# Performance work log

Hardware: AMD Instinct MI355X
Metric: run time of the kernel (lower is better)

Reference implementation:

```python
import jax, jax.numpy as jnp
import numpy as np

N_GLIMPSES = 3
GS = 64          # glimpse_size
IN_C = 3         # input_channels
B, H, W = 64, 512, 512


def get_glimpses(image, loc):
    """Multi-scale glimpse extraction (tf.image.extract_glimpse, centered+normalized)
    followed by antialiased bicubic resize to GS x GS, concatenated on channels."""
    b, h, w, c = image.shape
    max_size = GS * 2 ** (N_GLIMPSES - 1)
    padded = jnp.pad(image, ((0, 0), (max_size, max_size), (max_size, max_size), (0, 0)))
    hp, wp = h + 2 * max_size, w + 2 * max_size
    # normalized+centered offsets: (-1,-1)=upper-left, (1,1)=lower-right of padded image
    center = (loc + 1.0) * 0.5 * jnp.array([hp, wp], dtype=jnp.float32)  # (y, x) per batch
    glimpses = []
    for i in range(N_GLIMPSES):
        s = GS * 2 ** i  # current crop size (python int, static)
        tl = jnp.round(center - 0.5 * s).astype(jnp.int32)
        tl = jnp.clip(tl, 0, jnp.array([hp - s, wp - s], dtype=jnp.int32))

        def slice_one(img, yx):
            return jax.lax.dynamic_slice(img, (yx[0], yx[1], 0), (s, s, c))

        g = jax.vmap(slice_one)(padded, tl)                      # [B, s, s, C]
        g = jax.image.resize(g, (b, GS, GS, c), method='cubic')  # antialiased bicubic
        glimpses.append(g)
    return jnp.concatenate(glimpses, axis=-1)  # [B, GS, GS, N_GLIMPSES*C]


def setup_inputs() -> dict:
    key = jax.random.key(0)
    ks = jax.random.split(key, 10)
    image = jax.random.uniform(ks[0], (B, H, W, IN_C), dtype=jnp.float32)
    loc = jax.random.uniform(ks[1], (B, 2), dtype=jnp.float32, minval=-1.0, maxval=1.0)
    cg = N_GLIMPSES * IN_C
    # conv1_g: full-kernel (GS x GS) valid conv -> 1x1x128
    Wg = jax.random.normal(ks[2], (GS, GS, cg, 128), dtype=jnp.float32) * (1.0 / np.sqrt(GS * GS * cg))
    bg = jnp.zeros((128,), jnp.float32)
    # conv1_l: 1x1 conv on loc [B,1,1,2]
    Wl = jax.random.normal(ks[3], (2, 128), dtype=jnp.float32) * (1.0 / np.sqrt(2.0))
    bl = jnp.zeros((128,), jnp.float32)
    # out: 1x1 conv 128 -> 256
    Wo = jax.random.normal(ks[4], (128, 256), dtype=jnp.float32) * (1.0 / np.sqrt(128.0))
    bo = jnp.zeros((256,), jnp.float32)
    return {"image": image, "loc": loc, "Wg": Wg, "bg": bg, "Wl": Wl, "bl": bl, "Wo": Wo, "bo": bo}


def reference(image, loc, Wg, bg, Wl, bl, Wo, bo):
    glimpses = get_glimpses(image, loc)  # [B, GS, GS, N_GLIMPSES*IN_C]
    # conv1_g with kernel == glimpse size and VALID padding == dense contraction over hwc
    x1 = jax.nn.relu(jnp.einsum('bhwc,hwck->bk', glimpses, Wg) + bg)  # [B,128]
    x2 = jax.nn.relu(loc @ Wl + bl)                                   # [B,128]
    out = jax.nn.relu((x1 + x2) @ Wo + bo)                            # [B,256]
    return out
```

## Files before the change

kernel.cpp:

```cpp
#include <hip/hip_runtime.h>

#define IMG_H 512
#define IMG_W 512
#define PAD   256
#define HP    1024
#define BATCH 64
#define KTOT  36864
#define KTILE 144
#define KB    16
#define NTILES 256

__device__ __forceinline__ float keys_cubic(float x) {
  if (x >= 2.0f) return 0.0f;
  if (x >= 1.0f) return ((-0.5f * x + 2.5f) * x - 4.0f) * x + 2.0f;
  return ((1.5f * x - 2.5f) * x) * x + 1.0f;
}

template <int KS>
__device__ __forceinline__ void glimpse_resize_body(
    const float* __restrict__ imb, int b, int y, int tly, int tlx,
    float* __restrict__ G, int tid, float* tmp) {
  constexpr int S  = 64 * KS;
  constexpr int NT = 4 * KS;
  const float fks = (float)KS;

  float sy  = ((float)y + 0.5f) * fks - 0.5f;
  int   iy0 = (int)ceilf(sy - 2.0f * fks);
  float wy[NT];
  float wsum = 0.0f;
#pragma unroll
  for (int t = 0; t < NT; ++t) {
    int i = iy0 + t;
    float w = 0.0f;
    if (i >= 0 && i < S) w = keys_cubic(fabsf(sy - (float)i) / fks);
    wy[t] = w;
    wsum += w;
  }
  float winv = 1.0f / wsum;
#pragma unroll
  for (int t = 0; t < NT; ++t) wy[t] *= winv;

  for (int e = tid; e < S * 3; e += 256) {
    int xcol = e / 3;
    int c    = e - 3 * xcol;
    int px   = tlx - PAD + xcol;
    float a = 0.0f;
    if ((unsigned)px < (unsigned)IMG_W) {
      const float* colp = imb + (px * 3 + c);
#pragma unroll
      for (int t = 0; t < NT; ++t) {
        int py = tly + iy0 + t - PAD;
        if ((unsigned)py < (unsigned)IMG_H)
          a = fmaf(wy[t], colp[py * (IMG_W * 3)], a);
      }
    }
    tmp[e] = a;
  }
  __syncthreads();

  if (tid < 192) {
    int xo = tid / 3;
    int c  = tid - 3 * xo;
    float sx  = ((float)xo + 0.5f) * fks - 0.5f;
    int   ix0 = (int)ceilf(sx - 2.0f * fks);
    float a = 0.0f, wsx = 0.0f;
#pragma unroll
    for (int t = 0; t < NT; ++t) {
      int i = ix0 + t;
      if (i >= 0 && i < S) {
        float w = keys_cubic(fabsf(sx - (float)i) / fks);
        wsx += w;
        a = fmaf(w, tmp[i * 3 + c], a);
      }
    }
    constexpr int sc = (KS == 2) ? 1 : 2;
    G[(((size_t)b * 64 + y) * 64 + xo) * 9 + 3 * sc + c] = a / wsx;
  }
}

__global__ __launch_bounds__(256) void glimpse_kernel(
    const float* __restrict__ img, const float* __restrict__ loc,
    float* __restrict__ G) {
  __shared__ float tmp[768];
  int blk = blockIdx.x;
  int y   = blk & 63;
  int t3  = blk >> 6;
  int sc  = t3 % 3;
  int b   = t3 / 3;
  int tid = threadIdx.x;

  float cy = (loc[2 * b] + 1.0f) * 0.5f * 1024.0f;
  float cx = (loc[2 * b + 1] + 1.0f) * 0.5f * 1024.0f;
  int s   = 64 << sc;
  int tly = min(max((int)rintf(cy - 0.5f * (float)s), 0), HP - s);
  int tlx = min(max((int)rintf(cx - 0.5f * (float)s), 0), HP - s);
  const float* imb = img + (size_t)b * (IMG_H * IMG_W * 3);

  if (sc == 0) {
    if (tid < 192) {
      int x = tid / 3, c = tid - 3 * (tid / 3);
      int py = tly + y - PAD, px = tlx + x - PAD;
      float v = 0.0f;
      if ((unsigned)py < (unsigned)IMG_H && (unsigned)px < (unsigned)IMG_W)
        v = imb[(py * IMG_W + px) * 3 + c];
      G[(((size_t)b * 64 + y) * 64 + x) * 9 + c] = v;
    }
  } else if (sc == 1) {
    glimpse_resize_body<2>(imb, b, y, tly, tlx, G, tid, tmp);
  } else {
    glimpse_resize_body<4>(imb, b, y, tly, tlx, G, tid, tmp);
  }
}

__global__ __launch_bounds__(256) void gemm_kernel(
    const float* __restrict__ G, const float* __restrict__ Wg,
    float* __restrict__ partials) {
  const int tile = blockIdx.x;
  const int tid  = threadIdx.x;
  const int tn   = tid & 15;
  const int tm   = tid >> 4;
  __shared__ float Gs[2][KB][64];
  __shared__ float Ws[2][KB][128];

  const int gb = tid >> 2;
  const int gj = (tid & 3) * 4;
  const int wr = tid >> 4;
  const int wc = (tid & 15) * 8;
  const size_t gbase = (size_t)gb * KTOT + (size_t)tile * KTILE + gj;
  const size_t wbase = ((size_t)tile * KTILE + wr) * 128 + wc;

  float4 g4 = *(const float4*)(G + gbase);
  float4 wa = *(const float4*)(Wg + wbase);
  float4 wb = *(const float4*)(Wg + wbase + 4);

  float acc[4][8];
#pragma unroll
  for (int mi = 0; mi < 4; ++mi)
#pragma unroll
    for (int ni = 0; ni < 8; ++ni) acc[mi][ni] = 0.0f;

  constexpr int NCHUNK = KTILE / KB;
#pragma unroll
  for (int chunk = 0; chunk < NCHUNK; ++chunk) {
    const int buf = chunk & 1;
    Gs[buf][gj + 0][gb] = g4.x;
    Gs[buf][gj + 1][gb] = g4.y;
    Gs[buf][gj + 2][gb] = g4.z;
    Gs[buf][gj + 3][gb] = g4.w;
    *(float4*)&Ws[buf][wr][wc]     = wa;
    *(float4*)&Ws[buf][wr][wc + 4] = wb;
    __syncthreads();
    if (chunk + 1 < NCHUNK) {
      g4 = *(const float4*)(G + gbase + (chunk + 1) * KB);
      wa = *(const float4*)(Wg + wbase + (size_t)(chunk + 1) * KB * 128);
      wb = *(const float4*)(Wg + wbase + (size_t)(chunk + 1) * KB * 128 + 4);
    }
#pragma unroll
    for (int j = 0; j < KB; ++j) {
      float4 gv = *(const float4*)&Gs[buf][j][tm * 4];
      float4 w0 = *(const float4*)&Ws[buf][j][tn * 8];
      float4 w1 = *(const float4*)&Ws[buf][j][tn * 8 + 4];
      float gm[4] = {gv.x, gv.y, gv.z, gv.w};
      float wn[8] = {w0.x, w0.y, w0.z, w0.w, w1.x, w1.y, w1.z, w1.w};
#pragma unroll
      for (int mi = 0; mi < 4; ++mi)
#pragma unroll
        for (int ni = 0; ni < 8; ++ni)
          acc[mi][ni] = fmaf(gm[mi], wn[ni], acc[mi][ni]);
    }
  }

#pragma unroll
  for (int mi = 0; mi < 4; ++mi) {
    int m = tm * 4 + mi;
    float* dst = partials + ((size_t)m * NTILES + tile) * 128 + tn * 8;
    *(float4*)dst       = make_float4(acc[mi][0], acc[mi][1], acc[mi][2], acc[mi][3]);
    *(float4*)(dst + 4) = make_float4(acc[mi][4], acc[mi][5], acc[mi][6], acc[mi][7]);
  }
}

__global__ __launch_bounds__(256) void finalize_kernel(
    const float* __restrict__ partials, const float* __restrict__ loc,
    const float* __restrict__ bg, const float* __restrict__ Wl,
    const float* __restrict__ bl, const float* __restrict__ Wo,
    const float* __restrict__ bo, float* __restrict__ out) {
  int b   = blockIdx.x;
  int tid = threadIdx.x;
  int k    = tid & 127;
  int half = tid >> 7;

  const float* base = partials + (size_t)b * NTILES * 128;
  float s = 0.0f;
  for (int t = half; t < NTILES; t += 2)
    s += base[t * 128 + k];

  __shared__ float red[256];
  __shared__ float h[128];
  red[tid] = s;
  __syncthreads();
  if (tid < 128) {
    float ss = red[tid] + red[tid + 128];
    float x1 = fmaxf(ss + bg[tid], 0.0f);
    float x2 = fmaxf(fmaf(loc[2 * b], Wl[tid],
                          fmaf(loc[2 * b + 1], Wl[128 + tid], bl[tid])),
                     0.0f);
    h[tid] = x1 + x2;
  }
  __syncthreads();
  {
    int n = tid;
    float a = bo[n];
#pragma unroll 8
    for (int kk = 0; kk < 128; ++kk) a = fmaf(h[kk], Wo[kk * 256 + n], a);
    out[(size_t)b * 256 + n] = fmaxf(a, 0.0f);
  }
}

extern "C" void kernel_launch(void* const* d_in, const int* in_sizes, int n_in,
                              void* d_out, int out_size, void* d_ws, size_t ws_size,
                              hipStream_t stream) {
  const float* img = (const float*)d_in[0];
  const float* loc = (const float*)d_in[1];
  const float* Wg  = (const float*)d_in[2];
  const float* bg  = (const float*)d_in[3];
  const float* Wl  = (const float*)d_in[4];
  const float* bl  = (const float*)d_in[5];
  const float* Wo  = (const float*)d_in[6];
  const float* bo  = (const float*)d_in[7];
  float* out = (float*)d_out;

  float* ws = (float*)d_ws;
  float* G        = ws;
  float* partials = ws + 2359296;

  glimpse_kernel<<<BATCH * 3 * 64, 256, 0, stream>>>(img, loc, G);
  gemm_kernel<<<NTILES, 256, 0, stream>>>(G, Wg, partials);
  finalize_kernel<<<BATCH, 256, 0, stream>>>(partials, loc, bg, Wl, bl, Wo, bo, out);
}
```

Measured before the change: 344.1 us.

## Merge three glimpse scales into one block per row and vectorize finalize reduction

The glimpse kernel now handles all three scales for one (batch, row) in a single block instead of launching a separate block per scale. This cuts the block count threefold, shares the location and top-left computation, and keeps threads busy across scales that were previously imbalanced. The finalize kernel now reads the per-tile partial sums with float4 loads and reduces them in shared memory across 8 groups. In exchange, each glimpse block does more serial work and uses more shared memory, which may lower occupancy.

```diff
diff --git a/kernel.cpp b/kernel.cpp
--- a/kernel.cpp
+++ b/kernel.cpp
@@ -16,99 +16,138 @@
   return ((1.5f * x - 2.5f) * x) * x + 1.0f;
 }
 
-template <int KS>
-__device__ __forceinline__ void glimpse_resize_body(
-    const float* __restrict__ imb, int b, int y, int tly, int tlx,
-    float* __restrict__ G, int tid, float* tmp) {
-  constexpr int S  = 64 * KS;
-  constexpr int NT = 4 * KS;
-  const float fks = (float)KS;
-
-  float sy  = ((float)y + 0.5f) * fks - 0.5f;
-  int   iy0 = (int)ceilf(sy - 2.0f * fks);
-  float wy[NT];
-  float wsum = 0.0f;
-#pragma unroll
-  for (int t = 0; t < NT; ++t) {
-    int i = iy0 + t;
-    float w = 0.0f;
-    if (i >= 0 && i < S) w = keys_cubic(fabsf(sy - (float)i) / fks);
-    wy[t] = w;
-    wsum += w;
-  }
-  float winv = 1.0f / wsum;
-#pragma unroll
-  for (int t = 0; t < NT; ++t) wy[t] *= winv;
-
-  for (int e = tid; e < S * 3; e += 256) {
-    int xcol = e / 3;
-    int c    = e - 3 * xcol;
-    int px   = tlx - PAD + xcol;
+__device__ __forceinline__ int iclamp(int v, int lo, int hi) {
+  return min(max(v, lo), hi);
+}
+
+__global__ __launch_bounds__(256) void glimpse_kernel(
+    const float* __restrict__ img, const float* __restrict__ loc,
+    float* __restrict__ G) {
+  __shared__ float tmp1[384];
+  __shared__ float tmp2[768];
+  const int y   = blockIdx.x & 63;
+  const int b   = blockIdx.x >> 6;
+  const int tid = threadIdx.x;
+
+  const float cy = (loc[2 * b] + 1.0f) * 0.5f * 1024.0f;
+  const float cx = (loc[2 * b + 1] + 1.0f) * 0.5f * 1024.0f;
+  const int tly0 = iclamp((int)rintf(cy - 32.0f), 0, HP - 64);
+  const int tlx0 = iclamp((int)rintf(cx - 32.0f), 0, HP - 64);
+  const int tly1 = iclamp((int)rintf(cy - 64.0f), 0, HP - 128);
+  const int tlx1 = iclamp((int)rintf(cx - 64.0f), 0, HP - 128);
+  const int tly2 = iclamp((int)rintf(cy - 128.0f), 0, HP - 256);
+  const int tlx2 = iclamp((int)rintf(cx - 128.0f), 0, HP - 256);
+  const float* imb  = img + (size_t)b * (IMG_H * IMG_W * 3);
+  float*       Grow = G + ((size_t)b * 64 + y) * (64 * 9);
+
+  if (tid < 192) {
+    int x = tid / 3, c = tid - 3 * (tid / 3);
+    int py = tly0 + y - PAD, px = tlx0 + x - PAD;
+    float v = 0.0f;
+    if ((unsigned)py < (unsigned)IMG_H && (unsigned)px < (unsigned)IMG_W)
+      v = imb[(py * IMG_W + px) * 3 + c];
+    Grow[x * 9 + c] = v;
+  }
+
+  float wy1[8];
+  int iy0_1;
+  {
+    float sy = ((float)y + 0.5f) * 2.0f - 0.5f;
+    iy0_1 = (int)ceilf(sy - 4.0f);
+    float ws = 0.0f;
+#pragma unroll
+    for (int t = 0; t < 8; ++t) {
+      int i = iy0_1 + t;
+      float w = (i >= 0 && i < 128) ? keys_cubic(fabsf(sy - (float)i) * 0.5f) : 0.0f;
+      wy1[t] = w;
+      ws += w;
+    }
+    float wi = 1.0f / ws;
+#pragma unroll
+    for (int t = 0; t < 8; ++t) wy1[t] *= wi;
+  }
+  float wy2[16];
+  int iy0_2;
+  {
+    float sy = ((float)y + 0.5f) * 4.0f - 0.5f;
+    iy0_2 = (int)ceilf(sy - 8.0f);
+    float ws = 0.0f;
+#pragma unroll
+    for (int t = 0; t < 16; ++t) {
+      int i = iy0_2 + t;
+      float w = (i >= 0 && i < 256) ? keys_cubic(fabsf(sy - (float)i) * 0.25f) : 0.0f;
+      wy2[t] = w;
+      ws += w;
+    }
+    float wi = 1.0f / ws;
+#pragma unroll
+    for (int t = 0; t < 16; ++t) wy2[t] *= wi;
+  }
+
+  for (int e = tid; e < 384; e += 256) {
+    int x = e / 3, c = e - 3 * (e / 3);
+    int px = tlx1 - PAD + x;
     float a = 0.0f;
     if ((unsigned)px < (unsigned)IMG_W) {
       const float* colp = imb + (px * 3 + c);
 #pragma unroll
-      for (int t = 0; t < NT; ++t) {
-        int py = tly + iy0 + t - PAD;
+      for (int t = 0; t < 8; ++t) {
+        int py = tly1 + iy0_1 + t - PAD;
         if ((unsigned)py < (unsigned)IMG_H)
-          a = fmaf(wy[t], colp[py * (IMG_W * 3)], a);
-      }
-    }
-    tmp[e] = a;
+          a = fmaf(wy1[t], colp[py * (IMG_W * 3)], a);
+      }
+    }
+    tmp1[e] = a;
+  }
+  for (int e = tid; e < 768; e += 256) {
+    int x = e / 3, c = e - 3 * (e / 3);
+    int px = tlx2 - PAD + x;
+    float a = 0.0f;
+    if ((unsigned)px < (unsigned)IMG_W) {
+      const float* colp = imb + (px * 3 + c);
+#pragma unroll
+      for (int t = 0; t < 16; ++t) {
+        int py = tly2 + iy0_2 + t - PAD;
+        if ((unsigned)py < (unsigned)IMG_H)
+          a = fmaf(wy2[t], colp[py * (IMG_W * 3)], a);
+      }
+    }
+    tmp2[e] = a;
   }
   __syncthreads();
 
-  if (tid < 192) {
-    int xo = tid / 3;
-    int c  = tid - 3 * xo;
-    float sx  = ((float)xo + 0.5f) * fks - 0.5f;
-    int   ix0 = (int)ceilf(sx - 2.0f * fks);
-    float a = 0.0f, wsx = 0.0f;
-#pragma unroll
-    for (int t = 0; t < NT; ++t) {
-      int i = ix0 + t;
-      if (i >= 0 && i < S) {
-        float w = keys_cubic(fabsf(sx - (float)i) / fks);
-        wsx += w;
-        a = fmaf(w, tmp[i * 3 + c], a);
-      }
-    }
-    constexpr int sc = (KS == 2) ? 1 : 2;
-    G[(((size_t)b * 64 + y) * 64 + xo) * 9 + 3 * sc + c] = a / wsx;
-  }
-}
-
-__global__ __launch_bounds__(256) void glimpse_kernel(
-    const float* __restrict__ img, const float* __restrict__ loc,
-    float* __restrict__ G) {
-  __shared__ float tmp[768];
-  int blk = blockIdx.x;
-  int y   = blk & 63;
-  int t3  = blk >> 6;
-  int sc  = t3 % 3;
-  int b   = t3 / 3;
-  int tid = threadIdx.x;
-
-  float cy = (loc[2 * b] + 1.0f) * 0.5f * 1024.0f;
-  float cx = (loc[2 * b + 1] + 1.0f) * 0.5f * 1024.0f;
-  int s   = 64 << sc;
-  int tly = min(max((int)rintf(cy - 0.5f * (float)s), 0), HP - s);
-  int tlx = min(max((int)rintf(cx - 0.5f * (float)s), 0), HP - s);
-  const float* imb = img + (size_t)b * (IMG_H * IMG_W * 3);
-
-  if (sc == 0) {
-    if (tid < 192) {
-      int x = tid / 3, c = tid - 3 * (tid / 3);
-      int py = tly + y - PAD, px = tlx + x - PAD;
-      float v = 0.0f;
-      if ((unsigned)py < (unsigned)IMG_H && (unsigned)px < (unsigned)IMG_W)
-        v = imb[(py * IMG_W + px) * 3 + c];
-      G[(((size_t)b * 64 + y) * 64 + x) * 9 + c] = v;
-    }
-  } else if (sc == 1) {
-    glimpse_resize_body<2>(imb, b, y, tly, tlx, G, tid, tmp);
-  } else {
-    glimpse_resize_body<4>(imb, b, y, tly, tlx, G, tid, tmp);
+  for (int o = tid; o < 384; o += 256) {
+    int oo = (o >= 192) ? o - 192 : o;
+    int xo = oo / 3, c = oo - 3 * xo;
+    if (o < 192) {
+      float sx  = ((float)xo + 0.5f) * 2.0f - 0.5f;
+      int   ix0 = (int)ceilf(sx - 4.0f);
+      float a = 0.0f, wsx = 0.0f;
+#pragma unroll
+      for (int t = 0; t < 8; ++t) {
+        int i = ix0 + t;
+        if (i >= 0 && i < 128) {
+          float w = keys_cubic(fabsf(sx - (float)i) * 0.5f);
+          wsx += w;
+          a = fmaf(w, tmp1[i * 3 + c], a);
+        }
+      }
+      Grow[xo * 9 + 3 + c] = a / wsx;
+    } else {
+      float sx  = ((float)xo + 0.5f) * 4.0f - 0.5f;
+      int   ix0 = (int)ceilf(sx - 8.0f);
+      float a = 0.0f, wsx = 0.0f;
+#pragma unroll
+      for (int t = 0; t < 16; ++t) {
+        int i = ix0 + t;
+        if (i >= 0 && i < 256) {
+          float w = keys_cubic(fabsf(sx - (float)i) * 0.25f);
+          wsx += w;
+          a = fmaf(w, tmp2[i * 3 + c], a);
+        }
+      }
+      Grow[xo * 9 + 6 + c] = a / wsx;
+    }
   }
 }
 
@@ -184,22 +223,28 @@
     const float* __restrict__ bg, const float* __restrict__ Wl,
     const float* __restrict__ bl, const float* __restrict__ Wo,
     const float* __restrict__ bo, float* __restrict__ out) {
-  int b   = blockIdx.x;
-  int tid = threadIdx.x;
-  int k    = tid & 127;
-  int half = tid >> 7;
-
-  const float* base = partials + (size_t)b * NTILES * 128;
-  float s = 0.0f;
-  for (int t = half; t < NTILES; t += 2)
-    s += base[t * 128 + k];
-
-  __shared__ float red[256];
+  const int b   = blockIdx.x;
+  const int tid = threadIdx.x;
+
+  const float4* base = (const float4*)(partials + (size_t)b * NTILES * 128);
+  float4 acc = make_float4(0.f, 0.f, 0.f, 0.f);
+#pragma unroll 8
+  for (int i = 0; i < 32; ++i) {
+    float4 v = base[(size_t)i * 256 + tid];
+    acc.x += v.x; acc.y += v.y; acc.z += v.z; acc.w += v.w;
+  }
+
+  __shared__ float red[8][128];
   __shared__ float h[128];
-  red[tid] = s;
+  {
+    float* r = &red[tid >> 5][(tid & 31) * 4];
+    r[0] = acc.x; r[1] = acc.y; r[2] = acc.z; r[3] = acc.w;
+  }
   __syncthreads();
   if (tid < 128) {
-    float ss = red[tid] + red[tid + 128];
+    float ss = 0.0f;
+#pragma unroll
+    for (int g = 0; g < 8; ++g) ss += red[g][tid];
     float x1 = fmaxf(ss + bg[tid], 0.0f);
     float x2 = fmaxf(fmaf(loc[2 * b], Wl[tid],
                           fmaf(loc[2 * b + 1], Wl[128 + tid], bl[tid])),
@@ -233,7 +278,7 @@
   float* G        = ws;
   float* partials = ws + 2359296;
 
-  glimpse_kernel<<<BATCH * 3 * 64, 256, 0, stream>>>(img, loc, G);
+  glimpse_kernel<<<BATCH * 64, 256, 0, stream>>>(img, loc, G);
   gemm_kernel<<<NTILES, 256, 0, stream>>>(G, Wg, partials);
   finalize_kernel<<<BATCH, 256, 0, stream>>>(partials, loc, bg, Wl, bl, Wo, bo, out);
 }
```

Result: faster. 318.8 us (-7.3%).
